# Performance work log

Measured on AMD Instinct MI355X. Metric: run time of the kernel, lower is better.

Reference implementation:

```python
import jax, jax.numpy as jnp
import numpy as np

N, E, F_IN, HID, H, G = 50000, 800000, 128, 128, 4, 64
D = HID // H  # per-head dim = 32


def setup_inputs() -> dict:
    key = jax.random.key(0)
    ks = jax.random.split(key, 24)
    s = 0.05
    x = jax.random.normal(ks[0], (N, F_IN), dtype=jnp.float32)
    edge_index = jax.random.randint(ks[1], (2, E), 0, N, dtype=jnp.int64)
    batch = jnp.sort(jax.random.randint(ks[2], (N,), 0, G, dtype=jnp.int64))
    p = {}
    # layer 1: in F_IN -> H*D, layer 2: in HID -> H*D; each conv has q,k,v,skip linears (bias=True)
    names = ['Wq1', 'Wk1', 'Wv1', 'Ws1', 'Wq2', 'Wk2', 'Wv2', 'Ws2']
    dims = [(F_IN, HID)] * 4 + [(HID, HID)] * 4
    for i, (nm, dm) in enumerate(zip(names, dims)):
        p[nm] = jax.random.normal(ks[3 + 2 * i], dm, dtype=jnp.float32) * s
        p['b' + nm[1:]] = jax.random.normal(ks[4 + 2 * i], (dm[1],), dtype=jnp.float32) * s
    p['Wfc'] = jax.random.normal(ks[20], (HID, 1), dtype=jnp.float32) * s
    p['bfc'] = jax.random.normal(ks[21], (1,), dtype=jnp.float32) * s
    return {'x': x, 'edge_index': edge_index, 'batch': batch, **p}


def transformer_conv(x, edge_index, Wq, bq, Wk, bk, Wv, bv, Ws, bs):
    src, dst = edge_index[0], edge_index[1]  # messages flow src -> dst
    q = (x @ Wq + bq).reshape(-1, H, D)[dst]          # [E,H,D]
    k = (x @ Wk + bk).reshape(-1, H, D)[src]          # [E,H,D]
    v = (x @ Wv + bv).reshape(-1, H, D)[src]          # [E,H,D]
    logits = jnp.einsum('ehd,ehd->eh', q, k) / jnp.sqrt(jnp.float32(D))  # [E,H]
    m = jax.ops.segment_max(logits, dst, num_segments=N)                 # [N,H]
    e = jnp.exp(logits - m[dst])
    s = jax.ops.segment_sum(e, dst, num_segments=N)                      # [N,H]
    alpha = e / s[dst]
    agg = jax.ops.segment_sum(alpha[..., None] * v, dst, num_segments=N)  # [N,H,D]
    return agg.reshape(-1, HID) + (x @ Ws + bs)


def reference(x, edge_index, batch, Wq1, bq1, Wk1, bk1, Wv1, bv1, Ws1, bs1,
              Wq2, bq2, Wk2, bk2, Wv2, bv2, Ws2, bs2, Wfc, bfc):
    h = jax.nn.relu(transformer_conv(x, edge_index, Wq1, bq1, Wk1, bk1, Wv1, bv1, Ws1, bs1))
    h = jax.nn.relu(transformer_conv(h, edge_index, Wq2, bq2, Wk2, bk2, Wv2, bv2, Ws2, bs2))
    sums = jax.ops.segment_sum(h, batch, num_segments=G)                 # [G,HID]
    cnt = jax.ops.segment_sum(jnp.ones((h.shape[0],), h.dtype), batch, num_segments=G)
    pooled = sums / jnp.maximum(cnt, 1.0)[:, None]
    return (pooled @ Wfc + bfc).squeeze(-1)
```

## Files before the change

### kernel.cpp

```cpp
#include <hip/hip_runtime.h>
#include <hip/hip_bf16.h>
#include <math.h>

#define HID 128

typedef __attribute__((ext_vector_type(8))) short short8;
typedef __attribute__((ext_vector_type(4))) short short4v;
typedef __attribute__((ext_vector_type(4))) float f32x4;
typedef __attribute__((ext_vector_type(4))) int int4v;
typedef __attribute__((ext_vector_type(2))) unsigned int uint2v;
typedef __attribute__((ext_vector_type(4))) unsigned short ushort4v;
typedef __attribute__((ext_vector_type(2))) unsigned short ushort2v;
typedef __attribute__((ext_vector_type(2))) _Float16 half2v;

static inline size_t align256(size_t x){ return (x + 255) & ~(size_t)255; }

__device__ inline float bf2f(unsigned short h) {
  union { unsigned u; float f; } uf; uf.u = ((unsigned)h) << 16; return uf.f;
}
__device__ inline unsigned short f2bf(float f) {
  union { float f; unsigned u; } uf; uf.f = f;
  unsigned r = uf.u + 0x7fff + ((uf.u >> 16) & 1);
  return (unsigned short)(r >> 16);
}
__device__ inline unsigned short f2h(float f) {
  union { _Float16 h; unsigned short u; } c; c.h = (_Float16)f; return c.u;
}
__device__ inline half2v b2h2(unsigned u) {
  union { unsigned u; half2v h; } c; c.u = u; return c.h;
}

__device__ inline float dpp_rsum16(float x) {
  int v;
  v = __builtin_amdgcn_update_dpp(0, __float_as_int(x), 0xB1, 0xF, 0xF, true);
  x += __int_as_float(v);
  v = __builtin_amdgcn_update_dpp(0, __float_as_int(x), 0x4E, 0xF, 0xF, true);
  x += __int_as_float(v);
  v = __builtin_amdgcn_update_dpp(0, __float_as_int(x), 0x124, 0xF, 0xF, true);
  x += __int_as_float(v);
  v = __builtin_amdgcn_update_dpp(0, __float_as_int(x), 0x128, 0xF, 0xF, true);
  x += __int_as_float(v);
  return x;
}

__global__ __launch_bounds__(512) void k_prep(
    const float* W0, const float* W1, const float* W2, const float* W3,
    const float* W4, const float* W5, const float* W6, const float* W7,
    const float* b0, const float* b1, const float* b2, const float* b3,
    const float* b4, const float* b5, const float* b6, const float* b7,
    unsigned short* Wcat, float* Bcat,
    const int* __restrict__ edst, int* __restrict__ deg, int* __restrict__ rank, int e)
{
  __shared__ float tl[32][33];
  int t = threadIdx.x;
  if (blockIdx.x >= 128) {
    for (int i = (blockIdx.x - 128) * 512 + t; i < e; i += 512 * 512)
      rank[i] = atomicAdd(&deg[edst[i]], 1);
    return;
  }
  const float* Ws[8] = {W0, W1, W2, W3, W4, W5, W6, W7};
  const float* bs[8] = {b0, b1, b2, b3, b4, b5, b6, b7};
  int m = blockIdx.x >> 4, tile = blockIdx.x & 15;
  int tr = (tile >> 2) * 32, tc = (tile & 3) * 32;
  int tx = t & 31, ty = t >> 5;
  const float* Wm = Ws[m];
  #pragma unroll
  for (int r = 0; r < 32; r += 16) tl[ty + r][tx] = Wm[(tr + ty + r) * 128 + tc + tx];
  __syncthreads();
  #pragma unroll
  for (int r = 0; r < 32; r += 16)
    Wcat[m * 16384 + (tc + ty + r) * 128 + tr + tx] = f2bf(tl[tx][ty + r]);
  if (tile == 0 && t < 128) Bcat[m * 128 + t] = bs[m][t];
}

__global__ void k_scan_a(const int* __restrict__ deg, int* __restrict__ rowptr,
                         int* __restrict__ bsum, int n) {
  __shared__ int tmp[512];
  int t = threadIdx.x, i = blockIdx.x * 512 + t;
  int v = (i < n) ? deg[i] : 0;
  tmp[t] = v;
  __syncthreads();
  for (int off = 1; off < 512; off <<= 1) {
    int u = (t >= off) ? tmp[t - off] : 0;
    __syncthreads();
    tmp[t] += u;
    __syncthreads();
  }
  if (i < n) rowptr[i] = tmp[t] - v;
  if (t == 511) bsum[blockIdx.x] = tmp[t];
}

__global__ void k_scan_c(int* __restrict__ rowptr, const int* __restrict__ bsum,
                         int n, int e, int nb) {
  __shared__ int sred[8];
  __shared__ int base_sh;
  int t = threadIdx.x;
  int v = (t < nb && t < (int)blockIdx.x) ? bsum[t] : 0;
  #pragma unroll
  for (int off = 32; off >= 1; off >>= 1) v += __shfl_xor(v, off);
  if ((t & 63) == 0) sred[t >> 6] = v;
  __syncthreads();
  if (t == 0) {
    int b = 0;
    #pragma unroll
    for (int j = 0; j < 8; ++j) b += sred[j];
    base_sh = b;
  }
  __syncthreads();
  int i = blockIdx.x * 512 + t;
  if (i < n) rowptr[i] += base_sh;
  if (i == 0) rowptr[n] = e;
}

__global__ __launch_bounds__(256) void k_scatter(
    const int* __restrict__ esrc, const int* __restrict__ edst,
    const int* __restrict__ rowptr, const int* __restrict__ rank,
    int* __restrict__ csrc, int e)
{
  for (int i = blockIdx.x * 256 + threadIdx.x; i < e; i += gridDim.x * 256)
    csrc[rowptr[edst[i]] + rank[i]] = esrc[i] << 9;
}

template<int ABF16>
__global__ __launch_bounds__(256, 3) void k_qkvs(
    const void* __restrict__ Ain, const unsigned short* __restrict__ Wl,
    const float* __restrict__ Bl, unsigned short* __restrict__ Qb,
    unsigned short* __restrict__ KVb, unsigned short* __restrict__ Sb, int n)
{
  __shared__ unsigned short sA[64 * 128];
  __shared__ unsigned short sW[128 * 128];
  const int tid = threadIdx.x;
  const int rb = blockIdx.x * 64;
  const float QSC = 0.25503487f;

  if (ABF16) {
    const unsigned short* A = (const unsigned short*)Ain;
    #pragma unroll
    for (int it = 0; it < 4; ++it) {
      int q = tid + it * 256;
      int row = q >> 4, ch = q & 15;
      int gr = rb + row;
      short8 h = {0,0,0,0,0,0,0,0};
      if (gr < n) h = *reinterpret_cast<const short8*>(A + (size_t)gr * HID + ch * 8);
      *reinterpret_cast<short8*>(&sA[row * 128 + ((ch ^ (row & 7)) << 3)]) = h;
    }
  } else {
    const float* A = (const float*)Ain;
    #pragma unroll
    for (int it = 0; it < 8; ++it) {
      int q = tid + it * 256;
      int row = q >> 5, c4 = (q & 31) * 4;
      int gr = rb + row;
      f32x4 a = {0.f, 0.f, 0.f, 0.f};
      if (gr < n) a = *reinterpret_cast<const f32x4*>(A + (size_t)gr * HID + c4);
      short4v h;
      h.x = (short)f2bf(a.x); h.y = (short)f2bf(a.y);
      h.z = (short)f2bf(a.z); h.w = (short)f2bf(a.w);
      int eloff = row * 128 + (((c4 >> 3) ^ (row & 7)) << 3) + (c4 & 7);
      *reinterpret_cast<short4v*>(&sA[eloff]) = h;
    }
  }

  const int lane = tid & 63;
  const int wv = tid >> 6;

  auto stageW = [&](int y) {
    const unsigned short* Wy = Wl + (size_t)y * 16384;
    #pragma unroll
    for (int it = 0; it < 8; ++it) {
      int q = tid + it * 256;
      int c = q >> 4, ch = q & 15;
      short8 w = *reinterpret_cast<const short8*>(Wy + c * 128 + ch * 8);
      *reinterpret_cast<short8*>(&sW[c * 128 + ((ch ^ (c & 7)) << 3)]) = w;
    }
  };

  stageW(0);
  __syncthreads();

  short8 af[4];
  #pragma unroll
  for (int ks = 0; ks < 4; ++ks) {
    int ch = ks * 4 + (lane >> 4);
    int row = wv * 16 + (lane & 15);
    af[ks] = *reinterpret_cast<const short8*>(&sA[row * 128 + ((ch ^ (row & 7)) << 3)]);
  }

  f32x4 acc[8];
  auto compute = [&]() {
    #pragma unroll
    for (int mf = 0; mf < 8; ++mf) acc[mf] = (f32x4){0.f, 0.f, 0.f, 0.f};
    #pragma unroll
    for (int ks = 0; ks < 4; ++ks) {
      int ch = ks * 4 + (lane >> 4);
      short8 wf[8];
      #pragma unroll
      for (int mf = 0; mf < 8; ++mf) {
        int wc = mf * 16 + (lane & 15);
        wf[mf] = *reinterpret_cast<const short8*>(&sW[wc * 128 + ((ch ^ (wc & 7)) << 3)]);
      }
      #pragma unroll
      for (int mf = 0; mf < 8; ++mf)
        acc[mf] = __builtin_amdgcn_mfma_f32_16x16x32_bf16(wf[mf], af[ks], acc[mf], 0, 0, 0);
    }
  };

  const int gr = rb + wv * 16 + (lane & 15);
  const int cbase = (lane >> 4) << 2;

  compute();
  if (gr < n) {
    #pragma unroll
    for (int mf = 0; mf < 8; ++mf) {
      int c0 = mf * 16 + cbase;
      f32x4 b = *reinterpret_cast<const f32x4*>(Bl + 0 * 128 + c0);
      f32x4 v = acc[mf];
      ushort4v h;
      h.x = f2h((v.x + b.x) * QSC); h.y = f2h((v.y + b.y) * QSC);
      h.z = f2h((v.z + b.z) * QSC); h.w = f2h((v.w + b.w) * QSC);
      *reinterpret_cast<ushort4v*>(Qb + (size_t)gr * HID + c0) = h;
    }
  }

  __syncthreads();
  stageW(3);
  __syncthreads();
  compute();
  if (gr < n) {
    #pragma unroll
    for (int mf = 0; mf < 8; ++mf) {
      int c0 = mf * 16 + cbase;
      f32x4 b = *reinterpret_cast<const f32x4*>(Bl + 3 * 128 + c0);
      f32x4 v = acc[mf];
      ushort4v h;
      h.x = f2h(v.x + b.x); h.y = f2h(v.y + b.y);
      h.z = f2h(v.z + b.z); h.w = f2h(v.w + b.w);
      *reinterpret_cast<ushort4v*>(Sb + (size_t)gr * HID + c0) = h;
    }
  }

  __syncthreads();
  stageW(1);
  __syncthreads();
  compute();
  f32x4 kacc[8];
  #pragma unroll
  for (int mf = 0; mf < 8; ++mf) kacc[mf] = acc[mf];

  __syncthreads();
  stageW(2);
  __syncthreads();
  compute();
  if (gr < n) {
    #pragma unroll
    for (int mf = 0; mf < 8; ++mf) {
      int c0 = mf * 16 + cbase;
      f32x4 bk = *reinterpret_cast<const f32x4*>(Bl + 1 * 128 + c0);
      f32x4 bv = *reinterpret_cast<const f32x4*>(Bl + 2 * 128 + c0);
      f32x4 kv = kacc[mf], vv = acc[mf];
      short8 h;
      h[0] = (short)f2h(kv.x + bk.x); h[1] = (short)f2h(kv.y + bk.y);
      h[2] = (short)f2h(vv.x + bv.x); h[3] = (short)f2h(vv.y + bv.y);
      h[4] = (short)f2h(kv.z + bk.z); h[5] = (short)f2h(kv.w + bk.w);
      h[6] = (short)f2h(vv.z + bv.z); h[7] = (short)f2h(vv.w + bv.w);
      *reinterpret_cast<short8*>(KVb + (size_t)gr * 256 + 2 * c0) = h;
    }
  }
}

__global__ __launch_bounds__(256, 8) void k_attn2(
    const unsigned short* __restrict__ Qb, const unsigned short* __restrict__ KVb,
    const unsigned short* __restrict__ Sb, const int* __restrict__ rowptr,
    const int* __restrict__ csrc, unsigned short* __restrict__ Hout, int n)
{
  int wid = blockIdx.x * 4 + (threadIdx.x >> 6);
  if (wid >= n) return;
  int lane = threadIdx.x & 63;
  half2v qh = b2h2(*reinterpret_cast<const unsigned*>(Qb + (size_t)wid * HID + 2 * lane));
  int e0 = rowptr[wid], deg = rowptr[wid + 1] - e0;
  const int* cp = csrc + e0;
  const char* kvb = (const char*)KVb + lane * 8;
  float m = -INFINITY, s = 0.f, a0 = 0.f, a1 = 0.f;

  auto LDo = [&](int off) -> uint2v {
    return *reinterpret_cast<const uint2v*>(kvb + (unsigned)off);
  };
  auto proc1 = [&](uint2v kv) {
    float lg = dpp_rsum16(__builtin_amdgcn_fdot2(qh, b2h2(kv.x), 0.f, false));
    if (!__all(lg <= m + 11.5f)) {
      float nm = fmaxf(m, lg);
      float cc = __builtin_amdgcn_exp2f(m - nm);
      s *= cc; a0 *= cc; a1 *= cc; m = nm;
    }
    float p = __builtin_amdgcn_exp2f(lg - m);
    half2v vh = b2h2(kv.y);
    s += p;
    a0 = fmaf(p, (float)vh.x, a0);
    a1 = fmaf(p, (float)vh.y, a1);
  };
  auto proc4 = [&](uint2v e0v, uint2v e1v, uint2v e2v, uint2v e3v) {
    float l0 = dpp_rsum16(__builtin_amdgcn_fdot2(qh, b2h2(e0v.x), 0.f, false));
    float l1 = dpp_rsum16(__builtin_amdgcn_fdot2(qh, b2h2(e1v.x), 0.f, false));
    float l2 = dpp_rsum16(__builtin_amdgcn_fdot2(qh, b2h2(e2v.x), 0.f, false));
    float l3 = dpp_rsum16(__builtin_amdgcn_fdot2(qh, b2h2(e3v.x), 0.f, false));
    float qm = fmaxf(fmaxf(l0, l1), fmaxf(l2, l3));
    if (!__all(qm <= m + 11.5f)) {
      float nm = fmaxf(m, qm);
      float cc = __builtin_amdgcn_exp2f(m - nm);
      s *= cc; a0 *= cc; a1 *= cc; m = nm;
    }
    float p0 = __builtin_amdgcn_exp2f(l0 - m);
    float p1 = __builtin_amdgcn_exp2f(l1 - m);
    float p2 = __builtin_amdgcn_exp2f(l2 - m);
    float p3 = __builtin_amdgcn_exp2f(l3 - m);
    s += (p0 + p1) + (p2 + p3);
    half2v v0 = b2h2(e0v.y), v1 = b2h2(e1v.y), v2 = b2h2(e2v.y), v3 = b2h2(e3v.y);
    a0 = fmaf(p3, (float)v3.x, fmaf(p2, (float)v2.x, fmaf(p1, (float)v1.x, fmaf(p0, (float)v0.x, a0))));
    a1 = fmaf(p3, (float)v3.y, fmaf(p2, (float)v2.y, fmaf(p1, (float)v1.y, fmaf(p0, (float)v0.y, a1))));
  };

  int nq = deg >> 2, r = deg & 3;
  if (nq) {
    int4v o; __builtin_memcpy(&o, cp, 16);
    uint2v b0 = LDo(o.x), b1 = LDo(o.y), b2 = LDo(o.z), b3 = LDo(o.w);
    for (int q = 1; q < nq; ++q) {
      int4v no; __builtin_memcpy(&no, cp + 4 * q, 16);
      uint2v n0 = LDo(no.x), n1 = LDo(no.y), n2 = LDo(no.z), n3 = LDo(no.w);
      proc4(b0, b1, b2, b3);
      b0 = n0; b1 = n1; b2 = n2; b3 = n3;
    }
    proc4(b0, b1, b2, b3);
  }
  int tb = nq * 4;
  for (int i = 0; i < r; ++i) proc1(LDo(cp[tb + i]));

  float inv = (s > 0.f) ? 1.f / s : 0.f;
  half2v sh = b2h2(*reinterpret_cast<const unsigned*>(Sb + (size_t)wid * HID + 2 * lane));
  ushort2v h;
  h.x = f2bf(fmaxf(fmaf(a0, inv, (float)sh.x), 0.f));
  h.y = f2bf(fmaxf(fmaf(a1, inv, (float)sh.y), 0.f));
  *reinterpret_cast<ushort2v*>(Hout + (size_t)wid * HID + 2 * lane) = h;
}

__global__ __launch_bounds__(256) void k_poolfc(
    const unsigned short* __restrict__ H, const int* __restrict__ batch,
    const float* __restrict__ Wfc, const float* __restrict__ bfc,
    float* __restrict__ out, int n)
{
  int g = blockIdx.x;
  int lo = 0, hi = n;
  while (lo < hi) { int mid = (lo + hi) >> 1; if (batch[mid] < g) lo = mid + 1; else hi = mid; }
  int start = lo;
  hi = n;
  while (lo < hi) { int mid = (lo + hi) >> 1; if (batch[mid] < g + 1) lo = mid + 1; else hi = mid; }
  int end = lo;

  int t = threadIdx.x;
  int col = t & 127, rr = t >> 7;
  float a0 = 0.f, a1 = 0.f, a2 = 0.f, a3 = 0.f;
  int i = start + rr;
  for (; i + 6 < end; i += 8) {
    a0 += bf2f(H[(size_t)i * HID + col]);
    a1 += bf2f(H[(size_t)(i + 2) * HID + col]);
    a2 += bf2f(H[(size_t)(i + 4) * HID + col]);
    a3 += bf2f(H[(size_t)(i + 6) * HID + col]);
  }
  for (; i < end; i += 2) a0 += bf2f(H[(size_t)i * HID + col]);
  float v = ((a0 + a1) + (a2 + a3)) * Wfc[col];

  __shared__ float red[4];
  #pragma unroll
  for (int off = 32; off >= 1; off >>= 1) v += __shfl_xor(v, off);
  if ((t & 63) == 0) red[t >> 6] = v;
  __syncthreads();
  if (t == 0) {
    float tot = (red[0] + red[1]) + (red[2] + red[3]);
    float cnt = (float)(end - start);
    out[g] = tot / fmaxf(cnt, 1.f) + bfc[0];
  }
}

extern "C" void kernel_launch(void* const* d_in, const int* in_sizes, int n_in,
                              void* d_out, int out_size, void* d_ws, size_t ws_size,
                              hipStream_t stream)
{
  const float* x   = (const float*)d_in[0];
  const int*   ei  = (const int*)d_in[1];
  const int*   bat = (const int*)d_in[2];
  const float *Wq1 = (const float*)d_in[3],  *bq1 = (const float*)d_in[4];
  const float *Wk1 = (const float*)d_in[5],  *bk1 = (const float*)d_in[6];
  const float *Wv1 = (const float*)d_in[7],  *bv1 = (const float*)d_in[8];
  const float *Ws1 = (const float*)d_in[9],  *bs1 = (const float*)d_in[10];
  const float *Wq2 = (const float*)d_in[11], *bq2 = (const float*)d_in[12];
  const float *Wk2 = (const float*)d_in[13], *bk2 = (const float*)d_in[14];
  const float *Wv2 = (const float*)d_in[15], *bv2 = (const float*)d_in[16];
  const float *Ws2 = (const float*)d_in[17], *bs2 = (const float*)d_in[18];
  const float *Wfc = (const float*)d_in[19], *bfc = (const float*)d_in[20];
  float* out = (float*)d_out;

  const int N = in_sizes[0] / HID;
  const int E = in_sizes[1] / 2;
  const int G = 64;

  char* p = (char*)d_ws;
  auto alloc = [&](size_t bytes) -> char* { char* r = p; p += align256(bytes); return r; };
  unsigned short* Qb  = (unsigned short*)alloc((size_t)N * HID * 2);
  unsigned short* KVb = (unsigned short*)alloc((size_t)N * 256 * 2);
  unsigned short* Sb  = (unsigned short*)alloc((size_t)N * HID * 2);
  unsigned short* Hb  = (unsigned short*)alloc((size_t)N * HID * 2);
  unsigned short* H2b = (unsigned short*)alloc((size_t)N * HID * 2);
  unsigned short* Wcat = (unsigned short*)alloc((size_t)8 * 128 * 128 * 2);
  float* Bcat = (float*)alloc((size_t)8 * 128 * 4);
  int* rowptr = (int*)alloc((size_t)(N + 1) * sizeof(int));
  int* deg    = (int*)alloc((size_t)N * sizeof(int));
  int* rank   = (int*)alloc((size_t)E * sizeof(int));
  int* bsum   = (int*)alloc(4096);
  int* csrc   = (int*)alloc((size_t)E * sizeof(int));

  const int* esrc = ei;
  const int* edst = ei + E;

  hipMemsetAsync(deg, 0, (size_t)N * sizeof(int), stream);

  k_prep<<<640, 512, 0, stream>>>(
      Wq1, Wk1, Wv1, Ws1, Wq2, Wk2, Wv2, Ws2,
      bq1, bk1, bv1, bs1, bq2, bk2, bv2, bs2,
      Wcat, Bcat, edst, deg, rank, E);

  int SB = (N + 511) / 512;
  k_scan_a<<<SB, 512, 0, stream>>>(deg, rowptr, bsum, N);
  k_scan_c<<<SB, 512, 0, stream>>>(rowptr, bsum, N, E, SB);
  k_scatter<<<512, 256, 0, stream>>>(esrc, edst, rowptr, rank, csrc, E);

  int QB = (N + 63) / 64;
  k_qkvs<0><<<QB, 256, 0, stream>>>(x, Wcat, Bcat, Qb, KVb, Sb, N);
  k_attn2<<<(N + 3) / 4, 256, 0, stream>>>(Qb, KVb, Sb, rowptr, csrc, Hb, N);
  k_qkvs<1><<<QB, 256, 0, stream>>>(Hb, Wcat + 4 * 16384, Bcat + 512, Qb, KVb, Sb, N);
  k_attn2<<<(N + 3) / 4, 256, 0, stream>>>(Qb, KVb, Sb, rowptr, csrc, H2b, N);
  k_poolfc<<<G, 256, 0, stream>>>(H2b, bat, Wfc, bfc, out, N);
}
```

Before: 365.9 us.

## Fuse CSR build into cooperative kernel, double-buffer weights, deepen gather prefetch

Replaces the memset, prep, two scan kernels and scatter with one cooperative kernel that uses grid-wide syncs, removing several launches. The QKVS GEMM now double-buffers weight tiles in shared memory with register prefetch, lowering occupancy to 2 blocks. The attention kernel prefetches two groups of four neighbours ahead, with launch bounds reduced to 6. The pooling kernel reads packed bf16 pairs per row with wave-level partials. The cooperative launch adds grid-sync overhead and requires all 512 blocks to be co-resident.

```diff
diff --git a/kernel.cpp b/kernel.cpp
--- a/kernel.cpp
+++ b/kernel.cpp
@@ -1,6 +1,9 @@
 #include <hip/hip_runtime.h>
 #include <hip/hip_bf16.h>
+#include <hip/hip_cooperative_groups.h>
 #include <math.h>
+
+namespace cg = cooperative_groups;
 
 #define HID 128
 
@@ -43,96 +46,119 @@
   return x;
 }
 
-__global__ __launch_bounds__(512) void k_prep(
+__global__ __launch_bounds__(512) void k_csr(
     const float* W0, const float* W1, const float* W2, const float* W3,
     const float* W4, const float* W5, const float* W6, const float* W7,
     const float* b0, const float* b1, const float* b2, const float* b3,
     const float* b4, const float* b5, const float* b6, const float* b7,
     unsigned short* Wcat, float* Bcat,
-    const int* __restrict__ edst, int* __restrict__ deg, int* __restrict__ rank, int e)
+    const int* __restrict__ esrc, const int* __restrict__ edst,
+    int* __restrict__ deg, int* __restrict__ rank,
+    int* __restrict__ rowptr, int* __restrict__ bsum, int* __restrict__ csrc,
+    int e, int n)
 {
+  cg::grid_group grid = cg::this_grid();
   __shared__ float tl[32][33];
-  int t = threadIdx.x;
-  if (blockIdx.x >= 128) {
-    for (int i = (blockIdx.x - 128) * 512 + t; i < e; i += 512 * 512)
-      rank[i] = atomicAdd(&deg[edst[i]], 1);
-    return;
-  }
-  const float* Ws[8] = {W0, W1, W2, W3, W4, W5, W6, W7};
-  const float* bs[8] = {b0, b1, b2, b3, b4, b5, b6, b7};
-  int m = blockIdx.x >> 4, tile = blockIdx.x & 15;
-  int tr = (tile >> 2) * 32, tc = (tile & 3) * 32;
-  int tx = t & 31, ty = t >> 5;
-  const float* Wm = Ws[m];
-  #pragma unroll
-  for (int r = 0; r < 32; r += 16) tl[ty + r][tx] = Wm[(tr + ty + r) * 128 + tc + tx];
-  __syncthreads();
-  #pragma unroll
-  for (int r = 0; r < 32; r += 16)
-    Wcat[m * 16384 + (tc + ty + r) * 128 + tr + tx] = f2bf(tl[tx][ty + r]);
-  if (tile == 0 && t < 128) Bcat[m * 128 + t] = bs[m][t];
-}
-
-__global__ void k_scan_a(const int* __restrict__ deg, int* __restrict__ rowptr,
-                         int* __restrict__ bsum, int n) {
   __shared__ int tmp[512];
-  int t = threadIdx.x, i = blockIdx.x * 512 + t;
-  int v = (i < n) ? deg[i] : 0;
-  tmp[t] = v;
-  __syncthreads();
-  for (int off = 1; off < 512; off <<= 1) {
-    int u = (t >= off) ? tmp[t - off] : 0;
-    __syncthreads();
-    tmp[t] += u;
-    __syncthreads();
-  }
-  if (i < n) rowptr[i] = tmp[t] - v;
-  if (t == 511) bsum[blockIdx.x] = tmp[t];
-}
-
-__global__ void k_scan_c(int* __restrict__ rowptr, const int* __restrict__ bsum,
-                         int n, int e, int nb) {
   __shared__ int sred[8];
   __shared__ int base_sh;
-  int t = threadIdx.x;
-  int v = (t < nb && t < (int)blockIdx.x) ? bsum[t] : 0;
-  #pragma unroll
-  for (int off = 32; off >= 1; off >>= 1) v += __shfl_xor(v, off);
-  if ((t & 63) == 0) sred[t >> 6] = v;
-  __syncthreads();
-  if (t == 0) {
-    int b = 0;
-    #pragma unroll
-    for (int j = 0; j < 8; ++j) b += sred[j];
-    base_sh = b;
-  }
-  __syncthreads();
-  int i = blockIdx.x * 512 + t;
-  if (i < n) rowptr[i] += base_sh;
-  if (i == 0) rowptr[n] = e;
-}
-
-__global__ __launch_bounds__(256) void k_scatter(
-    const int* __restrict__ esrc, const int* __restrict__ edst,
-    const int* __restrict__ rowptr, const int* __restrict__ rank,
-    int* __restrict__ csrc, int e)
-{
-  for (int i = blockIdx.x * 256 + threadIdx.x; i < e; i += gridDim.x * 256)
+  const int t = threadIdx.x, bid = blockIdx.x;
+
+  if (bid < 128) {
+    const float* Ws[8] = {W0, W1, W2, W3, W4, W5, W6, W7};
+    const float* bs[8] = {b0, b1, b2, b3, b4, b5, b6, b7};
+    int m = bid >> 4, tile = bid & 15;
+    int tr = (tile >> 2) * 32, tc = (tile & 3) * 32;
+    int tx = t & 31, ty = t >> 5;
+    const float* Wm = Ws[m];
+    #pragma unroll
+    for (int r = 0; r < 32; r += 16) tl[ty + r][tx] = Wm[(tr + ty + r) * 128 + tc + tx];
+    __syncthreads();
+    #pragma unroll
+    for (int r = 0; r < 32; r += 16)
+      Wcat[m * 16384 + (tc + ty + r) * 128 + tr + tx] = f2bf(tl[tx][ty + r]);
+    if (tile == 0 && t < 128) Bcat[m * 128 + t] = bs[m][t];
+  } else {
+    for (int i = (bid - 128) * 512 + t; i < n; i += 384 * 512) deg[i] = 0;
+  }
+  grid.sync();
+
+  for (int i = bid * 512 + t; i < e; i += 512 * 512)
+    rank[i] = atomicAdd(&deg[edst[i]], 1);
+  grid.sync();
+
+  const int SB = (n + 511) >> 9;
+  if (bid < SB) {
+    int i = bid * 512 + t;
+    int v = (i < n) ? deg[i] : 0;
+    tmp[t] = v;
+    __syncthreads();
+    for (int off = 1; off < 512; off <<= 1) {
+      int u = (t >= off) ? tmp[t - off] : 0;
+      __syncthreads();
+      tmp[t] += u;
+      __syncthreads();
+    }
+    if (i < n) rowptr[i] = tmp[t] - v;
+    if (t == 511) bsum[bid] = tmp[t];
+  }
+  grid.sync();
+
+  if (bid < SB) {
+    int v = (t < SB && t < bid) ? bsum[t] : 0;
+    #pragma unroll
+    for (int off = 32; off >= 1; off >>= 1) v += __shfl_xor(v, off);
+    if ((t & 63) == 0) sred[t >> 6] = v;
+    __syncthreads();
+    if (t == 0) {
+      int b = 0;
+      #pragma unroll
+      for (int j = 0; j < 8; ++j) b += sred[j];
+      base_sh = b;
+    }
+    __syncthreads();
+    int i = bid * 512 + t;
+    if (i < n) rowptr[i] += base_sh;
+    if (i == 0) rowptr[n] = e;
+  }
+  grid.sync();
+
+  for (int i = bid * 512 + t; i < e; i += 512 * 512)
     csrc[rowptr[edst[i]] + rank[i]] = esrc[i] << 9;
 }
 
 template<int ABF16>
-__global__ __launch_bounds__(256, 3) void k_qkvs(
+__global__ __launch_bounds__(256, 2) void k_qkvs(
     const void* __restrict__ Ain, const unsigned short* __restrict__ Wl,
     const float* __restrict__ Bl, unsigned short* __restrict__ Qb,
     unsigned short* __restrict__ KVb, unsigned short* __restrict__ Sb, int n)
 {
   __shared__ unsigned short sA[64 * 128];
-  __shared__ unsigned short sW[128 * 128];
+  __shared__ unsigned short sW[2][128 * 128];
   const int tid = threadIdx.x;
   const int rb = blockIdx.x * 64;
   const float QSC = 0.25503487f;
 
+  short8 wreg[8];
+  auto loadW = [&](int y) {
+    const unsigned short* Wy = Wl + (size_t)y * 16384;
+    #pragma unroll
+    for (int it = 0; it < 8; ++it) {
+      int q = tid + it * 256;
+      wreg[it] = *reinterpret_cast<const short8*>(Wy + q * 8);
+    }
+  };
+  auto storeW = [&](unsigned short* buf) {
+    #pragma unroll
+    for (int it = 0; it < 8; ++it) {
+      int q = tid + it * 256;
+      int c = q >> 4, ch = q & 15;
+      *reinterpret_cast<short8*>(&buf[c * 128 + ((ch ^ (c & 7)) << 3)]) = wreg[it];
+    }
+  };
+
+  loadW(0);
+  storeW(sW[0]);
   if (ABF16) {
     const unsigned short* A = (const unsigned short*)Ain;
     #pragma unroll
@@ -160,23 +186,10 @@
       *reinterpret_cast<short4v*>(&sA[eloff]) = h;
     }
   }
+  __syncthreads();
 
   const int lane = tid & 63;
   const int wv = tid >> 6;
-
-  auto stageW = [&](int y) {
-    const unsigned short* Wy = Wl + (size_t)y * 16384;
-    #pragma unroll
-    for (int it = 0; it < 8; ++it) {
-      int q = tid + it * 256;
-      int c = q >> 4, ch = q & 15;
-      short8 w = *reinterpret_cast<const short8*>(Wy + c * 128 + ch * 8);
-      *reinterpret_cast<short8*>(&sW[c * 128 + ((ch ^ (c & 7)) << 3)]) = w;
-    }
-  };
-
-  stageW(0);
-  __syncthreads();
 
   short8 af[4];
   #pragma unroll
@@ -187,7 +200,7 @@
   }
 
   f32x4 acc[8];
-  auto compute = [&]() {
+  auto compute = [&](const unsigned short* buf) {
     #pragma unroll
     for (int mf = 0; mf < 8; ++mf) acc[mf] = (f32x4){0.f, 0.f, 0.f, 0.f};
     #pragma unroll
@@ -197,7 +210,7 @@
       #pragma unroll
       for (int mf = 0; mf < 8; ++mf) {
         int wc = mf * 16 + (lane & 15);
-        wf[mf] = *reinterpret_cast<const short8*>(&sW[wc * 128 + ((ch ^ (wc & 7)) << 3)]);
+        wf[mf] = *reinterpret_cast<const short8*>(&buf[wc * 128 + ((ch ^ (wc & 7)) << 3)]);
       }
       #pragma unroll
       for (int mf = 0; mf < 8; ++mf)
@@ -208,7 +221,8 @@
   const int gr = rb + wv * 16 + (lane & 15);
   const int cbase = (lane >> 4) << 2;
 
-  compute();
+  loadW(3);
+  compute(sW[0]);
   if (gr < n) {
     #pragma unroll
     for (int mf = 0; mf < 8; ++mf) {
@@ -221,11 +235,11 @@
       *reinterpret_cast<ushort4v*>(Qb + (size_t)gr * HID + c0) = h;
     }
   }
-
+  storeW(sW[1]);
   __syncthreads();
-  stageW(3);
-  __syncthreads();
-  compute();
+
+  loadW(1);
+  compute(sW[1]);
   if (gr < n) {
     #pragma unroll
     for (int mf = 0; mf < 8; ++mf) {
@@ -238,19 +252,18 @@
       *reinterpret_cast<ushort4v*>(Sb + (size_t)gr * HID + c0) = h;
     }
   }
-
+  storeW(sW[0]);
   __syncthreads();
-  stageW(1);
-  __syncthreads();
-  compute();
+
+  loadW(2);
+  compute(sW[0]);
   f32x4 kacc[8];
   #pragma unroll
   for (int mf = 0; mf < 8; ++mf) kacc[mf] = acc[mf];
-
+  storeW(sW[1]);
   __syncthreads();
-  stageW(2);
-  __syncthreads();
-  compute();
+
+  compute(sW[1]);
   if (gr < n) {
     #pragma unroll
     for (int mf = 0; mf < 8; ++mf) {
@@ -268,7 +281,7 @@
   }
 }
 
-__global__ __launch_bounds__(256, 8) void k_attn2(
+__global__ __launch_bounds__(256, 6) void k_attn2(
     const unsigned short* __restrict__ Qb, const unsigned short* __restrict__ KVb,
     const unsigned short* __restrict__ Sb, const int* __restrict__ rowptr,
     const int* __restrict__ csrc, unsigned short* __restrict__ Hout, int n)
@@ -320,16 +333,23 @@
   };
 
   int nq = deg >> 2, r = deg & 3;
-  if (nq) {
+  if (nq >= 2) {
+    int4v o0; __builtin_memcpy(&o0, cp, 16);
+    int4v o1; __builtin_memcpy(&o1, cp + 4, 16);
+    uint2v A0 = LDo(o0.x), A1 = LDo(o0.y), A2 = LDo(o0.z), A3 = LDo(o0.w);
+    uint2v B0 = LDo(o1.x), B1 = LDo(o1.y), B2 = LDo(o1.z), B3 = LDo(o1.w);
+    for (int q = 2; q < nq; ++q) {
+      int4v no; __builtin_memcpy(&no, cp + 4 * q, 16);
+      uint2v N0 = LDo(no.x), N1 = LDo(no.y), N2 = LDo(no.z), N3 = LDo(no.w);
+      proc4(A0, A1, A2, A3);
+      A0 = B0; A1 = B1; A2 = B2; A3 = B3;
+      B0 = N0; B1 = N1; B2 = N2; B3 = N3;
+    }
+    proc4(A0, A1, A2, A3);
+    proc4(B0, B1, B2, B3);
+  } else if (nq == 1) {
     int4v o; __builtin_memcpy(&o, cp, 16);
-    uint2v b0 = LDo(o.x), b1 = LDo(o.y), b2 = LDo(o.z), b3 = LDo(o.w);
-    for (int q = 1; q < nq; ++q) {
-      int4v no; __builtin_memcpy(&no, cp + 4 * q, 16);
-      uint2v n0 = LDo(no.x), n1 = LDo(no.y), n2 = LDo(no.z), n3 = LDo(no.w);
-      proc4(b0, b1, b2, b3);
-      b0 = n0; b1 = n1; b2 = n2; b3 = n3;
-    }
-    proc4(b0, b1, b2, b3);
+    proc4(LDo(o.x), LDo(o.y), LDo(o.z), LDo(o.w));
   }
   int tb = nq * 4;
   for (int i = 0; i < r; ++i) proc1(LDo(cp[tb + i]));
@@ -355,28 +375,24 @@
   while (lo < hi) { int mid = (lo + hi) >> 1; if (batch[mid] < g + 1) lo = mid + 1; else hi = mid; }
   int end = lo;
 
-  int t = threadIdx.x;
-  int col = t & 127, rr = t >> 7;
-  float a0 = 0.f, a1 = 0.f, a2 = 0.f, a3 = 0.f;
-  int i = start + rr;
-  for (; i + 6 < end; i += 8) {
-    a0 += bf2f(H[(size_t)i * HID + col]);
-    a1 += bf2f(H[(size_t)(i + 2) * HID + col]);
-    a2 += bf2f(H[(size_t)(i + 4) * HID + col]);
-    a3 += bf2f(H[(size_t)(i + 6) * HID + col]);
-  }
-  for (; i < end; i += 2) a0 += bf2f(H[(size_t)i * HID + col]);
-  float v = ((a0 + a1) + (a2 + a3)) * Wfc[col];
-
-  __shared__ float red[4];
-  #pragma unroll
-  for (int off = 32; off >= 1; off >>= 1) v += __shfl_xor(v, off);
-  if ((t & 63) == 0) red[t >> 6] = v;
+  int t = threadIdx.x, w = t >> 6, l = t & 63;
+  const unsigned* Hu = (const unsigned*)H;
+  float a0 = 0.f, a1 = 0.f;
+  for (int i = start + w; i < end; i += 4) {
+    unsigned u = Hu[(size_t)i * 64 + l];
+    a0 += bf2f((unsigned short)(u & 0xffff));
+    a1 += bf2f((unsigned short)(u >> 16));
+  }
+  __shared__ float part[4][64][2];
+  part[w][l][0] = a0; part[w][l][1] = a1;
   __syncthreads();
-  if (t == 0) {
-    float tot = (red[0] + red[1]) + (red[2] + red[3]);
-    float cnt = (float)(end - start);
-    out[g] = tot / fmaxf(cnt, 1.f) + bfc[0];
+  if (w == 0) {
+    float s0 = part[0][l][0] + part[1][l][0] + part[2][l][0] + part[3][l][0];
+    float s1 = part[0][l][1] + part[1][l][1] + part[2][l][1] + part[3][l][1];
+    float v = s0 * Wfc[2 * l] + s1 * Wfc[2 * l + 1];
+    #pragma unroll
+    for (int off = 32; off >= 1; off >>= 1) v += __shfl_xor(v, off);
+    if (l == 0) out[g] = v / fmaxf((float)(end - start), 1.f) + bfc[0];
   }
 }
 
@@ -420,17 +436,17 @@
   const int* esrc = ei;
   const int* edst = ei + E;
 
-  hipMemsetAsync(deg, 0, (size_t)N * sizeof(int), stream);
-
-  k_prep<<<640, 512, 0, stream>>>(
-      Wq1, Wk1, Wv1, Ws1, Wq2, Wk2, Wv2, Ws2,
-      bq1, bk1, bv1, bs1, bq2, bk2, bv2, bs2,
-      Wcat, Bcat, edst, deg, rank, E);
-
-  int SB = (N + 511) / 512;
-  k_scan_a<<<SB, 512, 0, stream>>>(deg, rowptr, bsum, N);
-  k_scan_c<<<SB, 512, 0, stream>>>(rowptr, bsum, N, E, SB);
-  k_scatter<<<512, 256, 0, stream>>>(esrc, edst, rowptr, rank, csrc, E);
+  void* cargs[] = {
+    (void*)&Wq1, (void*)&Wk1, (void*)&Wv1, (void*)&Ws1,
+    (void*)&Wq2, (void*)&Wk2, (void*)&Wv2, (void*)&Ws2,
+    (void*)&bq1, (void*)&bk1, (void*)&bv1, (void*)&bs1,
+    (void*)&bq2, (void*)&bk2, (void*)&bv2, (void*)&bs2,
+    (void*)&Wcat, (void*)&Bcat,
+    (void*)&esrc, (void*)&edst,
+    (void*)&deg, (void*)&rank, (void*)&rowptr, (void*)&bsum, (void*)&csrc,
+    (void*)&E, (void*)&N
+  };
+  hipLaunchCooperativeKernel((const void*)k_csr, dim3(512), dim3(512), cargs, 0, stream);
 
   int QB = (N + 63) / 64;
   k_qkvs<0><<<QB, 256, 0, stream>>>(x, Wcat, Bcat, Qb, KVb, Sb, N);
```

Result: slower. 643.5 us (+75.9%).
